# Optimization experiments

Measured on AMD Instinct MI355X. Metric: run time of the kernel, lower is better.

Reference implementation:

```python
import jax, jax.numpy as jnp
import numpy as np
from jax import lax

# Module hyperparameters (init_kwargs)
FH, FW = 5, 5          # kernel_size
DIL_Y, DIL_X = 2, 2    # kernel_dilation
G = 2                  # num_deform_groups
F = 64                 # filters
K = FH * FW            # kernel taps


def setup_inputs() -> dict:
    key = jax.random.key(0)
    ks = jax.random.split(key, 4)
    B, H, W, C = 4, 128, 128, 32
    volume = jax.random.normal(ks[0], (B, H, W, C), jnp.float32)
    # offset-predicting conv params: offset_num = FH*FW*G*2 = 100 channels
    w_off = jax.random.normal(ks[1], (FH, FW, C, K * 2 * G), jnp.float32) * 0.01
    b_off = jnp.zeros((K * 2 * G,), jnp.float32)
    # deformable conv weights: (taps, in_channels, filters)
    w_dcn = jax.random.normal(ks[2], (K, C, F), jnp.float32) * (1.0 / np.sqrt(K * C))
    b_dcn = jnp.zeros((F,), jnp.float32)
    return {"volume": volume, "w_off": w_off, "b_off": b_off,
            "w_dcn": w_dcn, "b_dcn": b_dcn}


def _deform_conv(volume, w_off, b_off, w_dcn, b_dcn):
    B, H, W, C = volume.shape
    dp_y = DIL_Y * (FH // 2)  # dilated_pad_y
    dp_x = DIL_X * (FW // 2)  # dilated_pad_x

    # 1) dense offset conv (VALID, dilated) -> (B, oh, ow, K*2*G)
    offsets = lax.conv_general_dilated(
        volume, w_off, window_strides=(1, 1), padding='VALID',
        rhs_dilation=(DIL_Y, DIL_X),
        dimension_numbers=('NHWC', 'HWIO', 'NHWC')) + b_off
    oh, ow = offsets.shape[1], offsets.shape[2]
    off = offsets.reshape(B, oh, ow, K, 2, G)  # [..., (dy,dx), group]

    # 2) base sampling grid (stride 1): output pixel centers + dilated taps
    base_y = jnp.arange(dp_y, H - dp_y, dtype=volume.dtype)   # (oh,)
    base_x = jnp.arange(dp_x, W - dp_x, dtype=volume.dtype)   # (ow,)
    kys = jnp.arange(-dp_y, dp_y + 1, DIL_Y, dtype=volume.dtype)
    kxs = jnp.arange(-dp_x, dp_x + 1, DIL_X, dtype=volume.dtype)
    kus, kvs = jnp.meshgrid(kxs, kys)         # (FH, FW) as in source
    kdy = kvs.reshape(-1)                     # (K,)
    kdx = kus.reshape(-1)                     # (K,)

    # sample positions: (B, oh, ow, K, G)
    py = base_y[None, :, None, None, None] + kdy[None, None, None, :, None] + off[..., 0, :]
    px = base_x[None, None, :, None, None] + kdx[None, None, None, :, None] + off[..., 1, :]
    py = jnp.clip(py, 0.0, H - 1.0)
    px = jnp.clip(px, 0.0, W - 1.0)

    # 3) bilinear gather
    y0 = jnp.clip(jnp.floor(py), 0.0, H - 2.0)
    x0 = jnp.clip(jnp.floor(px), 0.0, W - 2.0)
    wy = (py - y0)[..., None]
    wx = (px - x0)[..., None]
    y0i = y0.astype(jnp.int32)
    x0i = x0.astype(jnp.int32)
    bidx = jnp.arange(B)[:, None, None, None, None]

    def gather(yy, xx):
        return volume[bidx, yy, xx]  # (B, oh, ow, K, G, C)

    v00 = gather(y0i, x0i)
    v01 = gather(y0i, x0i + 1)
    v10 = gather(y0i + 1, x0i)
    v11 = gather(y0i + 1, x0i + 1)
    sampled = (v00 * (1 - wy) * (1 - wx) + v01 * (1 - wy) * wx
               + v10 * wy * (1 - wx) + v11 * wy * wx)  # (B, oh, ow, K, G, C)

    # 4) weighted conv; deform groups partition the output filters
    wr = w_dcn.reshape(K, C, G, F // G)
    out = jnp.einsum('bhwkgc,kcgf->bhwgf', sampled, wr).reshape(B, oh, ow, F)
    return out + b_dcn


def reference(volume, w_off, b_off, w_dcn, b_dcn):
    return _deform_conv(volume, w_off, b_off, w_dcn, b_dcn)
```

## Files before the change

kernel.cpp:

```cpp
#include <hip/hip_runtime.h>
#include <hip/hip_bf16.h>

#define BB 4
#define HH 128
#define WW 128
#define CC 32
#define OH 120
#define OW 120
#define KT 25
#define OFFC 100
#define FF 64
#define NPX 32
#define NTHREADS 512

typedef __attribute__((ext_vector_type(8))) short bf16x8;
typedef __attribute__((ext_vector_type(4))) float f32x4;

#define WB_ELEMS   (KT * 7 * 64 * 8)
#define WD_ELEMS   (4 * KT * 64 * 8)
#define VOL_UNITS  (BB * HH * WW * CC / 8)
#define VOL16_OFF  (WB_ELEMS + WD_ELEMS)

__device__ __forceinline__ short f2bf(float x) {
    __hip_bfloat16 h = __float2bfloat16(x);
    return *reinterpret_cast<short*>(&h);
}
__device__ __forceinline__ float asf(unsigned u) { return __uint_as_float(u); }

__global__ __launch_bounds__(256) void repack_kernel(
    const float* __restrict__ volume, const float* __restrict__ w_off,
    const float* __restrict__ w_dcn, short* __restrict__ ws)
{
    int idx = blockIdx.x * 256 + threadIdx.x;
    short* WB  = ws;
    short* WD  = ws + WB_ELEMS;
    short* V16 = ws + VOL16_OFF;
    if (idx < WB_ELEMS) {
        int j = idx & 7, l = (idx >> 3) & 63;
        int tn = idx >> 9;
        int n = tn % 7, t = tn / 7;
        int c = (l >> 4) * 8 + j;
        int oc = n * 16 + (l & 15);
        float v = (oc < OFFC) ? w_off[(t * CC + c) * OFFC + oc] : 0.f;
        WB[idx] = f2bf(v);
    } else if (idx < WB_ELEMS + WD_ELEMS) {
        int idx2 = idx - WB_ELEMS;
        int j = idx2 & 7, l = (idx2 >> 3) & 63;
        int nt = idx2 >> 9;
        int t = nt % KT, n = nt / KT;
        int c = (l >> 4) * 8 + j;
        int f = n * 16 + (l & 15);
        WD[idx2] = f2bf(w_dcn[(t * CC + c) * FF + f]);
    } else {
        int v = idx - (WB_ELEMS + WD_ELEMS);
        if (v < VOL_UNITS) {
            const float* src = volume + (size_t)v * 8;
            float4 q0 = *(const float4*)src;
            float4 q1 = *(const float4*)(src + 4);
            alignas(16) short tmp[8];
            tmp[0] = f2bf(q0.x); tmp[1] = f2bf(q0.y); tmp[2] = f2bf(q0.z); tmp[3] = f2bf(q0.w);
            tmp[4] = f2bf(q1.x); tmp[5] = f2bf(q1.y); tmp[6] = f2bf(q1.z); tmp[7] = f2bf(q1.w);
            *(bf16x8*)&V16[(size_t)v * 8] = *(const bf16x8*)tmp;
        }
    }
}

__global__ __launch_bounds__(512, 4) void dcn_fused(
    const short* __restrict__ ws_ro, const float* __restrict__ b_off,
    const float* __restrict__ b_dcn, float* __restrict__ out)
{
    __shared__ __align__(16) char smem[38528];
    short* patch   = (short*)smem;
    uint4* pos4    = (uint4*)smem;
    float* offtile = (float*)(smem + 25600);
    f32x4* red     = (f32x4*)(smem + 25600);

    const short* WB  = ws_ro;
    const short* WD  = ws_ro + WB_ELEMS;
    const short* V16 = ws_ro + VOL16_OFF;

    const int tid  = threadIdx.x;
    const int lane = tid & 63;
    const int wv   = tid >> 6;
    const int ox0  = blockIdx.x * NPX;
    const int oy   = blockIdx.y;
    const int b    = blockIdx.z;
    const short* Vb = V16 + (size_t)b * (HH * WW * CC);

    for (int i = tid; i < 9 * 40 * 4; i += NTHREADS) {
        int cq = i & 3;
        int xi = (i >> 2) % 40;
        int yi = (i >> 2) / 40;
        int col = ox0 + xi; col = (col < WW) ? col : (WW - 1);
        bf16x8 v = *(const bf16x8*)&Vb[((size_t)(oy + yi) * WW + col) * CC + cq * 8];
        int u = ((yi * 40 + xi) << 2) + (cq ^ (xi & 3) ^ ((xi >> 2) & 3));
        *(bf16x8*)&patch[u * 8] = v;
    }
    __syncthreads();

    if (wv < 7) {
        const int pr = lane & 15, cq = lane >> 4;
        f32x4 a0 = (f32x4){0.f, 0.f, 0.f, 0.f};
        f32x4 a1 = (f32x4){0.f, 0.f, 0.f, 0.f};
        for (int fh = 0; fh < 5; ++fh) {
            #pragma unroll
            for (int fw = 0; fw < 5; ++fw) {
                int t = fh * 5 + fw;
                int x0 = pr + 2 * fw, x1 = x0 + 16;
                bf16x8 af0 = *(const bf16x8*)&patch[((((2 * fh) * 40 + x0) << 2) + (cq ^ (x0 & 3) ^ ((x0 >> 2) & 3))) * 8];
                bf16x8 af1 = *(const bf16x8*)&patch[((((2 * fh) * 40 + x1) << 2) + (cq ^ (x1 & 3) ^ ((x1 >> 2) & 3))) * 8];
                bf16x8 bf = *(const bf16x8*)&WB[(t * 7 + wv) * 512 + lane * 8];
                a0 = __builtin_amdgcn_mfma_f32_16x16x32_bf16(af0, bf, a0, 0, 0, 0);
                a1 = __builtin_amdgcn_mfma_f32_16x16x32_bf16(af1, bf, a1, 0, 0, 0);
            }
        }
        int col = lane & 15, q = lane >> 4;
        int oc = wv * 16 + col;
        if (oc < OFFC) {
            float bo = b_off[oc];
            #pragma unroll
            for (int r = 0; r < 4; ++r) {
                offtile[(q * 4 + r) * 101 + oc]        = a0[r] + bo;
                offtile[(16 + q * 4 + r) * 101 + oc]   = a1[r] + bo;
            }
        }
    }
    __syncthreads();

    for (int item = tid; item < 1600; item += NTHREADS) {
        int p = item & 31, g = (item >> 5) & 1, t = item >> 6;
        int t5 = t / 5, tm5 = t - t5 * 5;
        float dy = offtile[p * 101 + t * 4 + g];
        float dx = offtile[p * 101 + t * 4 + 2 + g];
        float py = (float)(oy + 2 * t5) + dy;
        float px = (float)(ox0 + p + 2 * tm5) + dx;
        py = fminf(fmaxf(py, 0.f), 127.f);
        px = fminf(fmaxf(px, 0.f), 127.f);
        float y0f = fminf(floorf(py), 126.f);
        float x0f = fminf(floorf(px), 126.f);
        float wy = py - y0f, wx = px - x0f;
        int y0 = (int)y0f, x0i = (int)x0f;
        float w00 = (1.f - wy) * (1.f - wx);
        float w01 = (1.f - wy) * wx;
        float w10 = wy * (1.f - wx);
        float w11 = wy * wx;
        unsigned off = (unsigned)((y0 << 12) + (x0i << 5));
        unsigned wlo = ((unsigned)(unsigned short)f2bf(w00)) | (((unsigned)(unsigned short)f2bf(w01)) << 16);
        unsigned whi = ((unsigned)(unsigned short)f2bf(w10)) | (((unsigned)(unsigned short)f2bf(w11)) << 16);
        pos4[((t * 2 + g) << 5) + p] = make_uint4(off, wlo, whi, 0u);
    }
    __syncthreads();

    const int mt = wv >> 2, gg = (wv >> 1) & 1, th = wv & 1;
    const int t0 = th ? 13 : 0, t1 = th ? 25 : 13;
    const int p  = mt * 16 + (lane & 15);
    const int cq = lane >> 4;
    const short* vcq = Vb + cq * 8;
    const short* wd0 = WD + ((gg * 2 + 0) * KT) * 512 + lane * 8;
    const short* wd1 = WD + ((gg * 2 + 1) * KT) * 512 + lane * 8;
    f32x4 acc0 = (f32x4){0.f, 0.f, 0.f, 0.f};
    f32x4 acc1 = (f32x4){0.f, 0.f, 0.f, 0.f};

    uint4 pwA = pos4[((t0 * 2 + gg) << 5) + p];
    uint4 pwB = pos4[(((t0 + 1) * 2 + gg) << 5) + p];
    {
        const short* vb0 = vcq + pwA.x;
        uint4 cA = *(const uint4*)(vb0);
        uint4 cB = *(const uint4*)(vb0 + 32);
        uint4 cC = *(const uint4*)(vb0 + 4096);
        uint4 cD = *(const uint4*)(vb0 + 4128);
        for (int t = t0; t < t1; ++t) {
            int tp = (t + 2 < t1) ? (t + 2) : (t1 - 1);
            uint4 pwC = pos4[((tp * 2 + gg) << 5) + p];
            const short* vbN = vcq + pwB.x;
            uint4 nA = *(const uint4*)(vbN);
            uint4 nB = *(const uint4*)(vbN + 32);
            uint4 nC = *(const uint4*)(vbN + 4096);
            uint4 nD = *(const uint4*)(vbN + 4128);

            float w00 = asf(pwA.y << 16), w01 = asf(pwA.y & 0xffff0000u);
            float w10 = asf(pwA.z << 16), w11 = asf(pwA.z & 0xffff0000u);
            alignas(16) short tmp[8];
            #define COMB(au, bu, cu, du, k)                                          \
                {                                                                    \
                    float lo = asf((au) << 16) * w00 + asf((bu) << 16) * w01         \
                             + asf((cu) << 16) * w10 + asf((du) << 16) * w11;        \
                    float hi = asf((au) & 0xffff0000u) * w00 + asf((bu) & 0xffff0000u) * w01 \
                             + asf((cu) & 0xffff0000u) * w10 + asf((du) & 0xffff0000u) * w11; \
                    tmp[2 * (k)] = f2bf(lo); tmp[2 * (k) + 1] = f2bf(hi);            \
                }
            COMB(cA.x, cB.x, cC.x, cD.x, 0)
            COMB(cA.y, cB.y, cC.y, cD.y, 1)
            COMB(cA.z, cB.z, cC.z, cD.z, 2)
            COMB(cA.w, cB.w, cC.w, cD.w, 3)
            #undef COMB
            bf16x8 af = *(const bf16x8*)tmp;
            acc0 = __builtin_amdgcn_mfma_f32_16x16x32_bf16(af, *(const bf16x8*)&wd0[t * 512], acc0, 0, 0, 0);
            acc1 = __builtin_amdgcn_mfma_f32_16x16x32_bf16(af, *(const bf16x8*)&wd1[t * 512], acc1, 0, 0, 0);
            pwA = pwB; pwB = pwC;
            cA = nA; cB = nB; cC = nC; cD = nD;
        }
    }
    __syncthreads();

    if (th) {
        int slot = wv >> 1;
        red[(slot * 2 + 0) * 64 + lane] = acc0;
        red[(slot * 2 + 1) * 64 + lane] = acc1;
    }
    __syncthreads();
    if (!th) {
        int slot = wv >> 1;
        acc0 += red[(slot * 2 + 0) * 64 + lane];
        acc1 += red[(slot * 2 + 1) * 64 + lane];
        int col = lane & 15, q = lane >> 4;
        int f0 = (gg * 2 + 0) * 16 + col;
        int f1 = (gg * 2 + 1) * 16 + col;
        float bd0 = b_dcn[f0], bd1 = b_dcn[f1];
        long pix0 = ((long)b * OH + oy) * OW + ox0;
        #pragma unroll
        for (int r = 0; r < 4; ++r) {
            int pp = mt * 16 + q * 4 + r;
            if (ox0 + pp < OW) {
                out[(pix0 + pp) * FF + f0] = acc0[r] + bd0;
                out[(pix0 + pp) * FF + f1] = acc1[r] + bd1;
            }
        }
    }
}

extern "C" void kernel_launch(void* const* d_in, const int* in_sizes, int n_in,
                              void* d_out, int out_size, void* d_ws, size_t ws_size,
                              hipStream_t stream) {
    const float* volume = (const float*)d_in[0];
    const float* w_off  = (const float*)d_in[1];
    const float* b_off  = (const float*)d_in[2];
    const float* w_dcn  = (const float*)d_in[3];
    const float* b_dcn  = (const float*)d_in[4];
    float* out = (float*)d_out;
    short* ws  = (short*)d_ws;

    int repack_blocks = (WB_ELEMS + WD_ELEMS + VOL_UNITS + 255) / 256;
    repack_kernel<<<repack_blocks, 256, 0, stream>>>(volume, w_off, w_dcn, ws);

    dim3 g2((OW + NPX - 1) / NPX, OH, BB);
    dcn_fused<<<g2, NTHREADS, 0, stream>>>(ws, b_off, b_dcn, out);
}
```

Before: 152.7 us.

## Switch intermediates from bf16 to fp16 with packed-half bilinear blend

Converts the repacked volume and weights to fp16 and uses fp16 MFMA instructions. The bilinear blend now runs as packed half2 FMAs instead of unpacking bf16 to fp32, which cuts ALU work in the gather loop. The software pipeline that prefetched gather loads two taps ahead is removed and only position data is prefetched, so load latency may be more exposed. The repack kernel also has each thread convert four volume units, giving fewer threads, and fp16 changes the numeric range and precision.

New measurement: 153.1 us. Within noise of the previous version (+0.2%).

```diff
diff --git a/kernel.cpp b/kernel.cpp
--- a/kernel.cpp
+++ b/kernel.cpp
@@ -1,5 +1,6 @@
 #include <hip/hip_runtime.h>
 #include <hip/hip_bf16.h>
+#include <hip/hip_fp16.h>
 
 #define BB 4
 #define HH 128
@@ -13,19 +14,21 @@
 #define NPX 32
 #define NTHREADS 512
 
-typedef __attribute__((ext_vector_type(8))) short bf16x8;
-typedef __attribute__((ext_vector_type(4))) float f32x4;
+typedef __attribute__((ext_vector_type(8))) short   s16x8;
+typedef __attribute__((ext_vector_type(8))) _Float16 f16x8;
+typedef __attribute__((ext_vector_type(2))) _Float16 h2;
+typedef __attribute__((ext_vector_type(4))) float   f32x4;
 
 #define WB_ELEMS   (KT * 7 * 64 * 8)
 #define WD_ELEMS   (4 * KT * 64 * 8)
 #define VOL_UNITS  (BB * HH * WW * CC / 8)
+#define VOL_Q      (VOL_UNITS / 4)
 #define VOL16_OFF  (WB_ELEMS + WD_ELEMS)
 
-__device__ __forceinline__ short f2bf(float x) {
-    __hip_bfloat16 h = __float2bfloat16(x);
-    return *reinterpret_cast<short*>(&h);
-}
-__device__ __forceinline__ float asf(unsigned u) { return __uint_as_float(u); }
+__device__ __forceinline__ short f2h(float x) {
+    _Float16 h = (_Float16)x;
+    return __builtin_bit_cast(short, h);
+}
 
 __global__ __launch_bounds__(256) void repack_kernel(
     const float* __restrict__ volume, const float* __restrict__ w_off,
@@ -42,7 +45,7 @@
         int c = (l >> 4) * 8 + j;
         int oc = n * 16 + (l & 15);
         float v = (oc < OFFC) ? w_off[(t * CC + c) * OFFC + oc] : 0.f;
-        WB[idx] = f2bf(v);
+        WB[idx] = f2h(v);
     } else if (idx < WB_ELEMS + WD_ELEMS) {
         int idx2 = idx - WB_ELEMS;
         int j = idx2 & 7, l = (idx2 >> 3) & 63;
@@ -50,17 +53,21 @@
         int t = nt % KT, n = nt / KT;
         int c = (l >> 4) * 8 + j;
         int f = n * 16 + (l & 15);
-        WD[idx2] = f2bf(w_dcn[(t * CC + c) * FF + f]);
+        WD[idx2] = f2h(w_dcn[(t * CC + c) * FF + f]);
     } else {
-        int v = idx - (WB_ELEMS + WD_ELEMS);
-        if (v < VOL_UNITS) {
-            const float* src = volume + (size_t)v * 8;
-            float4 q0 = *(const float4*)src;
-            float4 q1 = *(const float4*)(src + 4);
-            alignas(16) short tmp[8];
-            tmp[0] = f2bf(q0.x); tmp[1] = f2bf(q0.y); tmp[2] = f2bf(q0.z); tmp[3] = f2bf(q0.w);
-            tmp[4] = f2bf(q1.x); tmp[5] = f2bf(q1.y); tmp[6] = f2bf(q1.z); tmp[7] = f2bf(q1.w);
-            *(bf16x8*)&V16[(size_t)v * 8] = *(const bf16x8*)tmp;
+        int v0 = idx - (WB_ELEMS + WD_ELEMS);
+        if (v0 < VOL_Q) {
+            #pragma unroll
+            for (int k = 0; k < 4; ++k) {
+                size_t v = (size_t)v0 + (size_t)k * VOL_Q;
+                const float* src = volume + v * 8;
+                float4 q0 = *(const float4*)src;
+                float4 q1 = *(const float4*)(src + 4);
+                alignas(16) short tmp[8];
+                tmp[0] = f2h(q0.x); tmp[1] = f2h(q0.y); tmp[2] = f2h(q0.z); tmp[3] = f2h(q0.w);
+                tmp[4] = f2h(q1.x); tmp[5] = f2h(q1.y); tmp[6] = f2h(q1.z); tmp[7] = f2h(q1.w);
+                *(s16x8*)&V16[v * 8] = *(const s16x8*)tmp;
+            }
         }
     }
 }
@@ -92,9 +99,9 @@
         int xi = (i >> 2) % 40;
         int yi = (i >> 2) / 40;
         int col = ox0 + xi; col = (col < WW) ? col : (WW - 1);
-        bf16x8 v = *(const bf16x8*)&Vb[((size_t)(oy + yi) * WW + col) * CC + cq * 8];
+        s16x8 v = *(const s16x8*)&Vb[((size_t)(oy + yi) * WW + col) * CC + cq * 8];
         int u = ((yi * 40 + xi) << 2) + (cq ^ (xi & 3) ^ ((xi >> 2) & 3));
-        *(bf16x8*)&patch[u * 8] = v;
+        *(s16x8*)&patch[u * 8] = v;
     }
     __syncthreads();
 
@@ -107,11 +114,11 @@
             for (int fw = 0; fw < 5; ++fw) {
                 int t = fh * 5 + fw;
                 int x0 = pr + 2 * fw, x1 = x0 + 16;
-                bf16x8 af0 = *(const bf16x8*)&patch[((((2 * fh) * 40 + x0) << 2) + (cq ^ (x0 & 3) ^ ((x0 >> 2) & 3))) * 8];
-                bf16x8 af1 = *(const bf16x8*)&patch[((((2 * fh) * 40 + x1) << 2) + (cq ^ (x1 & 3) ^ ((x1 >> 2) & 3))) * 8];
-                bf16x8 bf = *(const bf16x8*)&WB[(t * 7 + wv) * 512 + lane * 8];
-                a0 = __builtin_amdgcn_mfma_f32_16x16x32_bf16(af0, bf, a0, 0, 0, 0);
-                a1 = __builtin_amdgcn_mfma_f32_16x16x32_bf16(af1, bf, a1, 0, 0, 0);
+                f16x8 af0 = *(const f16x8*)&patch[((((2 * fh) * 40 + x0) << 2) + (cq ^ (x0 & 3) ^ ((x0 >> 2) & 3))) * 8];
+                f16x8 af1 = *(const f16x8*)&patch[((((2 * fh) * 40 + x1) << 2) + (cq ^ (x1 & 3) ^ ((x1 >> 2) & 3))) * 8];
+                f16x8 bf = *(const f16x8*)&WB[(t * 7 + wv) * 512 + lane * 8];
+                a0 = __builtin_amdgcn_mfma_f32_16x16x32_f16(af0, bf, a0, 0, 0, 0);
+                a1 = __builtin_amdgcn_mfma_f32_16x16x32_f16(af1, bf, a1, 0, 0, 0);
             }
         }
         int col = lane & 15, q = lane >> 4;
@@ -120,8 +127,8 @@
             float bo = b_off[oc];
             #pragma unroll
             for (int r = 0; r < 4; ++r) {
-                offtile[(q * 4 + r) * 101 + oc]        = a0[r] + bo;
-                offtile[(16 + q * 4 + r) * 101 + oc]   = a1[r] + bo;
+                offtile[(q * 4 + r) * 101 + oc]      = a0[r] + bo;
+                offtile[(16 + q * 4 + r) * 101 + oc] = a1[r] + bo;
             }
         }
     }
@@ -145,8 +152,8 @@
         float w10 = wy * (1.f - wx);
         float w11 = wy * wx;
         unsigned off = (unsigned)((y0 << 12) + (x0i << 5));
-        unsigned wlo = ((unsigned)(unsigned short)f2bf(w00)) | (((unsigned)(unsigned short)f2bf(w01)) << 16);
-        unsigned whi = ((unsigned)(unsigned short)f2bf(w10)) | (((unsigned)(unsigned short)f2bf(w11)) << 16);
+        unsigned wlo = ((unsigned)(unsigned short)f2h(w00)) | (((unsigned)(unsigned short)f2h(w01)) << 16);
+        unsigned whi = ((unsigned)(unsigned short)f2h(w10)) | (((unsigned)(unsigned short)f2h(w11)) << 16);
         pos4[((t * 2 + g) << 5) + p] = make_uint4(off, wlo, whi, 0u);
     }
     __syncthreads();
@@ -161,45 +168,44 @@
     f32x4 acc0 = (f32x4){0.f, 0.f, 0.f, 0.f};
     f32x4 acc1 = (f32x4){0.f, 0.f, 0.f, 0.f};
 
-    uint4 pwA = pos4[((t0 * 2 + gg) << 5) + p];
-    uint4 pwB = pos4[(((t0 + 1) * 2 + gg) << 5) + p];
-    {
-        const short* vb0 = vcq + pwA.x;
-        uint4 cA = *(const uint4*)(vb0);
-        uint4 cB = *(const uint4*)(vb0 + 32);
-        uint4 cC = *(const uint4*)(vb0 + 4096);
-        uint4 cD = *(const uint4*)(vb0 + 4128);
-        for (int t = t0; t < t1; ++t) {
-            int tp = (t + 2 < t1) ? (t + 2) : (t1 - 1);
-            uint4 pwC = pos4[((tp * 2 + gg) << 5) + p];
-            const short* vbN = vcq + pwB.x;
-            uint4 nA = *(const uint4*)(vbN);
-            uint4 nB = *(const uint4*)(vbN + 32);
-            uint4 nC = *(const uint4*)(vbN + 4096);
-            uint4 nD = *(const uint4*)(vbN + 4128);
-
-            float w00 = asf(pwA.y << 16), w01 = asf(pwA.y & 0xffff0000u);
-            float w10 = asf(pwA.z << 16), w11 = asf(pwA.z & 0xffff0000u);
-            alignas(16) short tmp[8];
-            #define COMB(au, bu, cu, du, k)                                          \
-                {                                                                    \
-                    float lo = asf((au) << 16) * w00 + asf((bu) << 16) * w01         \
-                             + asf((cu) << 16) * w10 + asf((du) << 16) * w11;        \
-                    float hi = asf((au) & 0xffff0000u) * w00 + asf((bu) & 0xffff0000u) * w01 \
-                             + asf((cu) & 0xffff0000u) * w10 + asf((du) & 0xffff0000u) * w11; \
-                    tmp[2 * (k)] = f2bf(lo); tmp[2 * (k) + 1] = f2bf(hi);            \
-                }
-            COMB(cA.x, cB.x, cC.x, cD.x, 0)
-            COMB(cA.y, cB.y, cC.y, cD.y, 1)
-            COMB(cA.z, cB.z, cC.z, cD.z, 2)
-            COMB(cA.w, cB.w, cC.w, cD.w, 3)
-            #undef COMB
-            bf16x8 af = *(const bf16x8*)tmp;
-            acc0 = __builtin_amdgcn_mfma_f32_16x16x32_bf16(af, *(const bf16x8*)&wd0[t * 512], acc0, 0, 0, 0);
-            acc1 = __builtin_amdgcn_mfma_f32_16x16x32_bf16(af, *(const bf16x8*)&wd1[t * 512], acc1, 0, 0, 0);
-            pwA = pwB; pwB = pwC;
-            cA = nA; cB = nB; cC = nC; cD = nD;
-        }
+    uint4 pw = pos4[((t0 * 2 + gg) << 5) + p];
+    for (int t = t0; t < t1; ++t) {
+        int tn = (t + 1 < t1) ? t + 1 : t0;
+        uint4 pwN = pos4[((tn * 2 + gg) << 5) + p];
+
+        const short* vb0 = vcq + pw.x;
+        uint4 Au = *(const uint4*)(vb0);
+        uint4 Bu = *(const uint4*)(vb0 + CC);
+        uint4 Cu = *(const uint4*)(vb0 + WW * CC);
+        uint4 Du = *(const uint4*)(vb0 + WW * CC + CC);
+
+        unsigned wyv = pw.y, wzv = pw.z;
+        unsigned u00 = ((wyv & 0xffffu) << 16) | (wyv & 0xffffu);
+        unsigned u01 = (wyv & 0xffff0000u) | (wyv >> 16);
+        unsigned u10 = ((wzv & 0xffffu) << 16) | (wzv & 0xffffu);
+        unsigned u11 = (wzv & 0xffff0000u) | (wzv >> 16);
+        h2 W00 = __builtin_bit_cast(h2, u00);
+        h2 W01 = __builtin_bit_cast(h2, u01);
+        h2 W10 = __builtin_bit_cast(h2, u10);
+        h2 W11 = __builtin_bit_cast(h2, u11);
+
+        alignas(16) unsigned tmpu[4];
+        #pragma unroll
+        for (int j = 0; j < 4; ++j) {
+            h2 a2 = __builtin_bit_cast(h2, ((const unsigned*)&Au)[j]);
+            h2 b2 = __builtin_bit_cast(h2, ((const unsigned*)&Bu)[j]);
+            h2 c2 = __builtin_bit_cast(h2, ((const unsigned*)&Cu)[j]);
+            h2 d2 = __builtin_bit_cast(h2, ((const unsigned*)&Du)[j]);
+            h2 r = a2 * W00;
+            r = __builtin_elementwise_fma(b2, W01, r);
+            r = __builtin_elementwise_fma(c2, W10, r);
+            r = __builtin_elementwise_fma(d2, W11, r);
+            tmpu[j] = __builtin_bit_cast(unsigned, r);
+        }
+        f16x8 af = *(const f16x8*)tmpu;
+        acc0 = __builtin_amdgcn_mfma_f32_16x16x32_f16(af, *(const f16x8*)&wd0[t * 512], acc0, 0, 0, 0);
+        acc1 = __builtin_amdgcn_mfma_f32_16x16x32_f16(af, *(const f16x8*)&wd1[t * 512], acc1, 0, 0, 0);
+        pw = pwN;
     }
     __syncthreads();
 
@@ -240,7 +246,8 @@
     float* out = (float*)d_out;
     short* ws  = (short*)d_ws;
 
-    int repack_blocks = (WB_ELEMS + WD_ELEMS + VOL_UNITS + 255) / 256;
+    int repack_threads = WB_ELEMS + WD_ELEMS + VOL_Q;
+    int repack_blocks  = (repack_threads + 255) / 256;
     repack_kernel<<<repack_blocks, 256, 0, stream>>>(volume, w_off, w_dcn, ws);
 
     dim3 g2((OW + NPX - 1) / NPX, OH, BB);
```
